# Kernel optimization log

Measured on AMD Instinct MI355X. Metric: run time of the kernel, lower is better.

## Reference

```python
import jax, jax.numpy as jnp
import numpy as np

N, E, G, P = 65536, 1048576, 512, 128   # nodes, edges, graphs, nodes per graph
K = 64                                   # sort-pool k (fixed in module)
NUM_CLASSES = 10
FEAT = 128


def _gcn_conv(x, W, b, src, dst):
    # PyG GCNConv: linear, add self-loops, symmetric-normalized aggregation, bias
    h = x @ W
    deg = jnp.ones((N,), x.dtype).at[dst].add(1.0)       # self-loop + in-degree
    dinv = jax.lax.rsqrt(deg)
    coef = (dinv[src] * dinv[dst])[:, None]
    agg = jax.ops.segment_sum(h[src] * coef, dst, num_segments=N)
    agg = agg + h * (dinv * dinv)[:, None]               # self-loop messages
    return agg + b


def setup_inputs() -> dict:
    key = jax.random.key(0)
    ks = jax.random.split(key, 12)
    x = jax.random.normal(ks[0], (N, FEAT), jnp.float32)
    src = jax.random.randint(ks[1], (E,), 0, N, dtype=jnp.int32)
    off = jax.random.randint(ks[2], (E,), 0, P, dtype=jnp.int32)
    dst = (src // P) * P + off                           # keep edges intra-graph
    edge_index = jnp.stack([src, dst])
    # balanced batch vector (implicit): node n belongs to graph n // P
    def lin(k, i, o):
        return jax.random.normal(k, (i, o), jnp.float32) / np.float32(np.sqrt(i))
    return {
        "x": x,
        "W1": lin(ks[3], FEAT, 128), "b1": jnp.zeros((128,), jnp.float32),
        "W2": lin(ks[4], 128, 64),   "b2": jnp.zeros((64,), jnp.float32),
        "W3": lin(ks[5], 64, 32),    "b3": jnp.zeros((32,), jnp.float32),
        "W4": lin(ks[6], 32, 32),    "b4": jnp.zeros((32,), jnp.float32),
        "W5": lin(ks[7], 256, 16).T, "b5": jnp.zeros((16,), jnp.float32),   # Conv1d(1,16,256,256)
        "W6": jax.random.normal(ks[8], (32, 16, 5), jnp.float32) * 0.1,      # Conv1d(16,32,5) OIH
        "b6": jnp.zeros((32,), jnp.float32),
        "Wf1": lin(ks[9], 896, 128), "bf1": jnp.zeros((128,), jnp.float32),
        "Wf2": lin(ks[10], 128, NUM_CLASSES), "bf2": jnp.zeros((NUM_CLASSES,), jnp.float32),
        "edge_index": edge_index,
    }


def reference(x, W1, b1, W2, b2, W3, b3, W4, b4, W5, b5, W6, b6,
              Wf1, bf1, Wf2, bf2, edge_index):
    src, dst = edge_index[0], edge_index[1]
    x1 = jnp.tanh(_gcn_conv(x, W1, b1, src, dst))
    x2 = jnp.tanh(_gcn_conv(x1, W2, b2, src, dst))
    x3 = jnp.tanh(_gcn_conv(x2, W3, b3, src, dst))
    x4 = jnp.tanh(_gcn_conv(x3, W4, b4, src, dst))
    h = jnp.concatenate([x1, x2, x3, x4], axis=-1)       # [N, 256]
    C = h.shape[-1]
    # global_sort_pool: balanced graphs of P nodes -> sort desc by last channel, take top-K
    hg = h.reshape(G, P, C)
    order = jnp.argsort(-hg[:, :, -1], axis=1)[:, :K]    # [G, K]
    pooled = jnp.take_along_axis(hg, order[:, :, None], axis=1)   # [G, K, C]
    # Conv1d(1, 16, 256, stride=256): kernel == stride == C, so per-node matmul
    z = jnp.einsum('gtj,cj->gct', pooled, W5) + b5[None, :, None]  # [G,16,64]
    z = jax.nn.relu(z)
    z = z.reshape(G, 16, -1, 2).max(axis=-1)                       # MaxPool1d(2,2) -> [G,16,32]
    z = jax.lax.conv_general_dilated(z, W6, (1,), 'VALID',
                                     dimension_numbers=('NCH', 'OIH', 'NCH'))
    z = jax.nn.relu(z + b6[None, :, None])                          # [G,32,28]
    z = z.reshape(G, -1)                                            # [G,896]
    out = jax.nn.relu(z @ Wf1 + bf1)
    # dropout is identity at eval time
    return jax.nn.log_softmax(out @ Wf2 + bf2, axis=-1)
```

## Files before the change

kernel.cpp:

```cpp
#include <hip/hip_runtime.h>

#define N_EDGES 1048576
#define N_GRAPH 512
#define REG     2560
#define MAXE    2560
#define PAD     64
#define CHUNK   4096

typedef __attribute__((ext_vector_type(4))) float floatx4;
typedef __attribute__((ext_vector_type(4))) int intx4;

__global__ void zero_kernel(unsigned* __restrict__ p, int n) {
    int i = blockIdx.x * blockDim.x + threadIdx.x;
    if (i < n) p[i] = 0u;
}

__global__ void scatter1p_kernel(const int* __restrict__ src, const int* __restrict__ dst,
                                 unsigned* __restrict__ cnt, unsigned short* __restrict__ ebuf) {
    __shared__ unsigned lhist[512];
    __shared__ unsigned lbase[512];
    int t = threadIdx.x;
    lhist[t] = 0; lhist[t + 256] = 0;
    __syncthreads();
    const intx4* s4 = (const intx4*)(src + blockIdx.x * CHUNK);
    const intx4* d4 = (const intx4*)(dst + blockIdx.x * CHUNK);
    unsigned gg[16]; unsigned short pk[16]; unsigned rr[16];
    int m = 0;
    for (int i = t; i < CHUNK / 4; i += 256) {
        intx4 sv = s4[i], dv = d4[i];
        int ss[4] = {sv.x, sv.y, sv.z, sv.w};
        int dd[4] = {dv.x, dv.y, dv.z, dv.w};
#pragma unroll
        for (int j = 0; j < 4; ++j) {
            unsigned g = ((unsigned)dd[j]) >> 7;
            gg[m] = g;
            pk[m] = (unsigned short)((ss[j] & 127) | ((dd[j] & 127) << 8));
            rr[m] = atomicAdd(&lhist[g], 1u);
            ++m;
        }
    }
    __syncthreads();
    lbase[t]       = lhist[t]       ? atomicAdd(&cnt[(size_t)t * PAD],         lhist[t])       : 0u;
    lbase[t + 256] = lhist[t + 256] ? atomicAdd(&cnt[(size_t)(t + 256) * PAD], lhist[t + 256]) : 0u;
    __syncthreads();
#pragma unroll
    for (int j = 0; j < 16; ++j) {
        unsigned pos = lbase[gg[j]] + rr[j];
        if (pos < REG) ebuf[(size_t)gg[j] * REG + pos] = pk[j];
    }
}

template<int CIN, int COUT>
__device__ void gcn_layer(const float* Xin, float* Xio,
                          const float* __restrict__ W, const float* __restrict__ Bv,
                          const float* __restrict__ dinv, const int* __restrict__ offs,
                          const unsigned char* __restrict__ csr,
                          const float* __restrict__ ecoef, int tid)
{
    constexpr int CL  = COUT / 4;
    constexpr int NPT = CL / 8;
    const int grp = tid / CL, cl = tid % CL;

    float acc[NPT][4];
#pragma unroll
    for (int ni = 0; ni < NPT; ++ni)
#pragma unroll
        for (int j = 0; j < 4; ++j) acc[ni][j] = 0.f;

    for (int k = 0; k < CIN; k += 4) {
        floatx4 xv[NPT];
#pragma unroll
        for (int ni = 0; ni < NPT; ++ni)
            xv[ni] = *(const floatx4*)(Xin + (grp * NPT + ni) * CIN + k);
#pragma unroll
        for (int i = 0; i < 4; ++i) {
            floatx4 wv = *(const floatx4*)(W + (k + i) * COUT + cl * 4);
#pragma unroll
            for (int ni = 0; ni < NPT; ++ni)
#pragma unroll
                for (int j = 0; j < 4; ++j)
                    acc[ni][j] += xv[ni][i] * wv[j];
        }
    }
    __syncthreads();
#pragma unroll
    for (int ni = 0; ni < NPT; ++ni) {
        floatx4 v; v[0] = acc[ni][0]; v[1] = acc[ni][1]; v[2] = acc[ni][2]; v[3] = acc[ni][3];
        *(floatx4*)(Xio + (grp * NPT + ni) * COUT + cl * 4) = v;
    }
    __syncthreads();

    floatx4 bv = *(const floatx4*)(Bv + cl * 4);
    float vout[NPT][4];
#pragma unroll
    for (int ni = 0; ni < NPT; ++ni) {
        int n = grp * NPT + ni;
        float dn = dinv[n];
        float a[4] = {0.f, 0.f, 0.f, 0.f};
        int o0 = offs[n], o1 = offs[n + 1];
        for (int p = o0; p < o1; ++p) {
            int s = csr[p] & 127;
            float cf = ecoef[p];
            floatx4 h = *(const floatx4*)(Xio + s * COUT + cl * 4);
#pragma unroll
            for (int j = 0; j < 4; ++j) a[j] += h[j] * cf;
        }
        float dnn = dn * dn;
#pragma unroll
        for (int j = 0; j < 4; ++j) {
            float t2 = a[j] + acc[ni][j] * dnn + bv[j];
            t2 = tanhf(t2);
            vout[ni][j] = fminf(fmaxf(t2, -1.0f), 1.0f);
        }
    }
    __syncthreads();
#pragma unroll
    for (int ni = 0; ni < NPT; ++ni) {
        floatx4 v; v[0] = vout[ni][0]; v[1] = vout[ni][1]; v[2] = vout[ni][2]; v[3] = vout[ni][3];
        *(floatx4*)(Xio + (grp * NPT + ni) * COUT + cl * 4) = v;
    }
    __syncthreads();
}

__global__ __launch_bounds__(1024, 1) void mega_kernel(
    const float* __restrict__ x,
    const float* __restrict__ W1, const float* __restrict__ b1,
    const float* __restrict__ W2, const float* __restrict__ b2,
    const float* __restrict__ W3, const float* __restrict__ b3,
    const float* __restrict__ W4, const float* __restrict__ b4,
    const float* __restrict__ W5, const float* __restrict__ b5,
    const float* __restrict__ W6, const float* __restrict__ b6,
    const float* __restrict__ Wf1, const float* __restrict__ bf1,
    const float* __restrict__ Wf2, const float* __restrict__ bf2,
    const unsigned* __restrict__ cnt, const unsigned short* __restrict__ ebuf,
    float* __restrict__ out)
{
    __shared__ __align__(16) char pool[157952];
    int*   ldeg = (int*)(pool + 0);
    int*   offs = (int*)(pool + 512);
    float* dinv = (float*)(pool + 1040);
    float* key  = (float*)(pool + 1552);
    unsigned short* ord = (unsigned short*)(pool + 2064);
    unsigned char*  csr = (unsigned char*)(pool + 2304);
    float* ecoef = (float*)(pool + 2304 + 2560 + 16);
    float* W5s   = (float*)(pool + 2304);
    float* X1   = (float*)(pool + 18688);
    float* X2   = (float*)(pool + 84224);
    float* X3   = (float*)(pool + 116992);
    float* X4   = (float*)(pool + 133376);
    float* SCR  = (float*)(pool + 149760);
    float* Zs   = SCR;
    float* ZMP  = SCR + 1024;
    float* Z896 = SCR;
    float* PART = SCR + 1024;
    float* FC1  = SCR + 896;
    float* LG   = SCR;

    const int g   = blockIdx.x;
    const int tid = threadIdx.x;
    int cnt_g = (int)cnt[(size_t)g * PAD];
    if (cnt_g > MAXE) cnt_g = MAXE;
    const unsigned short* eg = ebuf + (size_t)g * REG;

    unsigned short ev[3]; int ne = 0;
    for (int e = tid; e < cnt_g; e += 1024) ev[ne++] = eg[e];

    if (tid < 128) ldeg[tid] = 0;
    __syncthreads();
    for (int i = 0; i < ne; ++i) atomicAdd(&ldeg[(ev[i] >> 8) & 127], 1);
    __syncthreads();
    if (tid < 128) offs[tid + 1] = ldeg[tid];
    if (tid == 0)  offs[0] = 0;
    __syncthreads();
    for (int d = 1; d < 128; d <<= 1) {
        int v = 0;
        if (tid < 128 && tid >= d) v = offs[tid + 1 - d];
        __syncthreads();
        if (tid < 128 && tid >= d) offs[tid + 1] += v;
        __syncthreads();
    }
    if (tid < 128) {
        dinv[tid] = 1.0f / sqrtf((float)(1 + ldeg[tid]));
        ldeg[tid] = offs[tid];
    }
    __syncthreads();
    for (int i = 0; i < ne; ++i) {
        int dn_ = (ev[i] >> 8) & 127, sn = ev[i] & 127;
        int p = atomicAdd(&ldeg[dn_], 1);
        csr[p]   = (unsigned char)sn;
        ecoef[p] = dinv[sn] * dinv[dn_];
    }
    const float* xg = x + (size_t)g * 16384;
    for (int idx = tid; idx < 4096; idx += 1024)
        *(floatx4*)(X1 + idx * 4) = *(const floatx4*)(xg + idx * 4);
    __syncthreads();

    gcn_layer<128, 128>(X1, X1, W1, b1, dinv, offs, csr, ecoef, tid);
    gcn_layer<128,  64>(X1, X2, W2, b2, dinv, offs, csr, ecoef, tid);
    gcn_layer< 64,  32>(X2, X3, W3, b3, dinv, offs, csr, ecoef, tid);
    gcn_layer< 32,  32>(X3, X4, W4, b4, dinv, offs, csr, ecoef, tid);

    if (tid < 128) key[tid] = X4[tid * 32 + 31];
    if (tid < 64)  ord[tid] = (unsigned short)tid;
    __syncthreads();
    for (int idx = tid; idx < 4096; idx += 1024) W5s[idx] = W5[idx];
    __syncthreads();
    if (tid < 128) {
        float myk = key[tid];
        int r = 0;
        for (int j = 0; j < 128; ++j) {
            float kj = key[j];
            r += (kj > myk) || (kj == myk && j < tid);
        }
        if (r < 64) ord[r] = (unsigned short)tid;
    }
    __syncthreads();

    {
        int q = tid >> 6, t = tid & 63;
        int node = ord[t] & 127;
        float z0 = b5[q];
        const float* w5a = W5s + q * 256;
        floatx4 zv = {0.f, 0.f, 0.f, 0.f};
        for (int jj = 0; jj < 32; ++jj) {
            int j = (jj + t) & 31;
            floatx4 pv = *(const floatx4*)(X1 + node * 128 + j * 4);
            floatx4 wv = *(const floatx4*)(w5a + j * 4);
#pragma unroll
            for (int u = 0; u < 4; ++u) zv[u] += pv[u] * wv[u];
        }
        for (int jj = 0; jj < 16; ++jj) {
            int j = (jj + t) & 15;
            floatx4 pv = *(const floatx4*)(X2 + node * 64 + j * 4);
            floatx4 wv = *(const floatx4*)(w5a + 128 + j * 4);
#pragma unroll
            for (int u = 0; u < 4; ++u) zv[u] += pv[u] * wv[u];
        }
        for (int jj = 0; jj < 8; ++jj) {
            int j = (jj + t) & 7;
            floatx4 pv = *(const floatx4*)(X3 + node * 32 + j * 4);
            floatx4 wv = *(const floatx4*)(w5a + 192 + j * 4);
#pragma unroll
            for (int u = 0; u < 4; ++u) zv[u] += pv[u] * wv[u];
        }
        for (int jj = 0; jj < 8; ++jj) {
            int j = (jj + t) & 7;
            floatx4 pv = *(const floatx4*)(X4 + node * 32 + j * 4);
            floatx4 wv = *(const floatx4*)(w5a + 224 + j * 4);
#pragma unroll
            for (int u = 0; u < 4; ++u) zv[u] += pv[u] * wv[u];
        }
        z0 += zv[0] + zv[1] + zv[2] + zv[3];
        Zs[q * 64 + t] = fmaxf(z0, 0.f);
    }
    __syncthreads();
    if (tid < 512) {
        int c = tid >> 5, p = tid & 31;
        ZMP[c * 32 + p] = fmaxf(Zs[c * 64 + 2 * p], Zs[c * 64 + 2 * p + 1]);
    }
    __syncthreads();
    for (int idx = tid; idx < 2560; idx += 1024) W5s[idx] = W6[idx];
    __syncthreads();
    if (tid < 896) {
        int oc = tid / 28, p = tid % 28;
        float s = b6[oc];
#pragma unroll
        for (int i = 0; i < 16; ++i) {
            const float* wrow = W5s + (oc * 16 + i) * 5;
#pragma unroll
            for (int k = 0; k < 5; ++k)
                s += ZMP[i * 32 + p + k] * wrow[k];
        }
        Z896[tid] = fmaxf(s, 0.f);
    }
    __syncthreads();
    {
        int f = tid & 127, q = tid >> 7;
        float s = 0.f;
        for (int i = q * 112; i < (q + 1) * 112; ++i)
            s += Z896[i] * Wf1[i * 128 + f];
        PART[q * 128 + f] = s;
    }
    __syncthreads();
    if (tid < 128) {
        float s = bf1[tid];
#pragma unroll
        for (int q = 0; q < 8; ++q) s += PART[q * 128 + tid];
        FC1[tid] = fmaxf(s, 0.f);
    }
    __syncthreads();
    if (tid < 10) {
        float s = bf2[tid];
        for (int i = 0; i < 128; ++i) s += FC1[i] * Wf2[i * 10 + tid];
        LG[tid] = s;
    }
    __syncthreads();
    if (tid == 0) {
        float mx = LG[0];
        for (int i = 1; i < 10; ++i) mx = fmaxf(mx, LG[i]);
        float se = 0.f;
        for (int i = 0; i < 10; ++i) se += expf(LG[i] - mx);
        LG[16] = mx + logf(se);
    }
    __syncthreads();
    if (tid < 10)
        out[g * 10 + tid] = LG[tid] - LG[16];
}

extern "C" void kernel_launch(void* const* d_in, const int* in_sizes, int n_in,
                              void* d_out, int out_size, void* d_ws, size_t ws_size,
                              hipStream_t stream) {
    (void)in_sizes; (void)n_in; (void)out_size; (void)ws_size;
    const float* x   = (const float*)d_in[0];
    const float* W1  = (const float*)d_in[1];
    const float* b1  = (const float*)d_in[2];
    const float* W2  = (const float*)d_in[3];
    const float* b2  = (const float*)d_in[4];
    const float* W3  = (const float*)d_in[5];
    const float* b3  = (const float*)d_in[6];
    const float* W4  = (const float*)d_in[7];
    const float* b4  = (const float*)d_in[8];
    const float* W5  = (const float*)d_in[9];
    const float* b5  = (const float*)d_in[10];
    const float* W6  = (const float*)d_in[11];
    const float* b6  = (const float*)d_in[12];
    const float* Wf1 = (const float*)d_in[13];
    const float* bf1 = (const float*)d_in[14];
    const float* Wf2 = (const float*)d_in[15];
    const float* bf2 = (const float*)d_in[16];
    const int* ei  = (const int*)d_in[17];
    const int* src = ei;
    const int* dst = ei + N_EDGES;

    char* ws = (char*)d_ws;
    unsigned* cnt         = (unsigned*)(ws);
    unsigned short* ebuf  = (unsigned short*)(ws + 131072);

    zero_kernel<<<32, 1024, 0, stream>>>(cnt, 512 * PAD);
    scatter1p_kernel<<<N_EDGES / CHUNK, 256, 0, stream>>>(src, dst, cnt, ebuf);
    mega_kernel<<<N_GRAPH, 1024, 0, stream>>>(x, W1, b1, W2, b2, W3, b3, W4, b4,
                                              W5, b5, W6, b6, Wf1, bf1, Wf2, bf2,
                                              cnt, ebuf, (float*)d_out);
}
```

Before: 285.3 us.

## Split GCN layer into matmul and agg phases, stage scatter writes in LDS

The scatter kernel now processes smaller chunks, does a local prefix scan per chunk, and stages packed edges in shared memory so the global writes to the per-graph edge buffers go out grouped by graph. In the mega kernel each GCN layer is split into a matmul phase and an aggregation phase. Aggregation is remapped so each thread owns one node and a contiguous channel slice, and the edge coefficient and source index are packed into a single float2 load. This is meant to cut scattered global stores and balance per-thread aggregation work. The cost is more shared memory and more barriers, and some threads sit idle in the narrow aggregation layers.

```diff
diff --git a/kernel.cpp b/kernel.cpp
--- a/kernel.cpp
+++ b/kernel.cpp
@@ -5,9 +5,11 @@
 #define REG     2560
 #define MAXE    2560
 #define PAD     64
-#define CHUNK   4096
+#define CHUNK   2048
+#define SBLK    (N_EDGES / CHUNK)
 
 typedef __attribute__((ext_vector_type(4))) float floatx4;
+typedef __attribute__((ext_vector_type(2))) float floatx2;
 typedef __attribute__((ext_vector_type(4))) int intx4;
 
 __global__ void zero_kernel(unsigned* __restrict__ p, int n) {
@@ -15,50 +17,66 @@
     if (i < n) p[i] = 0u;
 }
 
-__global__ void scatter1p_kernel(const int* __restrict__ src, const int* __restrict__ dst,
-                                 unsigned* __restrict__ cnt, unsigned short* __restrict__ ebuf) {
+__global__ void scatter_kernel(const int* __restrict__ src, const int* __restrict__ dst,
+                               unsigned* __restrict__ cnt, unsigned short* __restrict__ ebuf) {
+    __shared__ unsigned short sbuf[CHUNK];
+    __shared__ unsigned short sg[CHUNK];
     __shared__ unsigned lhist[512];
-    __shared__ unsigned lbase[512];
-    int t = threadIdx.x;
+    __shared__ unsigned lscan[512];
+    __shared__ unsigned gbase[512];
+    const int t = threadIdx.x;
     lhist[t] = 0; lhist[t + 256] = 0;
     __syncthreads();
-    const intx4* s4 = (const intx4*)(src + blockIdx.x * CHUNK);
-    const intx4* d4 = (const intx4*)(dst + blockIdx.x * CHUNK);
-    unsigned gg[16]; unsigned short pk[16]; unsigned rr[16];
-    int m = 0;
-    for (int i = t; i < CHUNK / 4; i += 256) {
-        intx4 sv = s4[i], dv = d4[i];
+    const intx4* s4 = (const intx4*)(src + blockIdx.x * CHUNK) + t * 2;
+    const intx4* d4 = (const intx4*)(dst + blockIdx.x * CHUNK) + t * 2;
+    unsigned short gg[8], pk[8], rr[8];
+#pragma unroll
+    for (int h = 0; h < 2; ++h) {
+        intx4 sv = s4[h], dv = d4[h];
         int ss[4] = {sv.x, sv.y, sv.z, sv.w};
         int dd[4] = {dv.x, dv.y, dv.z, dv.w};
 #pragma unroll
         for (int j = 0; j < 4; ++j) {
             unsigned g = ((unsigned)dd[j]) >> 7;
-            gg[m] = g;
-            pk[m] = (unsigned short)((ss[j] & 127) | ((dd[j] & 127) << 8));
-            rr[m] = atomicAdd(&lhist[g], 1u);
-            ++m;
-        }
-    }
-    __syncthreads();
-    lbase[t]       = lhist[t]       ? atomicAdd(&cnt[(size_t)t * PAD],         lhist[t])       : 0u;
-    lbase[t + 256] = lhist[t + 256] ? atomicAdd(&cnt[(size_t)(t + 256) * PAD], lhist[t + 256]) : 0u;
-    __syncthreads();
-#pragma unroll
-    for (int j = 0; j < 16; ++j) {
-        unsigned pos = lbase[gg[j]] + rr[j];
-        if (pos < REG) ebuf[(size_t)gg[j] * REG + pos] = pk[j];
+            gg[h * 4 + j] = (unsigned short)g;
+            pk[h * 4 + j] = (unsigned short)((ss[j] & 127) | ((dd[j] & 127) << 8));
+            rr[h * 4 + j] = (unsigned short)atomicAdd(&lhist[g], 1u);
+        }
+    }
+    __syncthreads();
+    unsigned a0 = lhist[t], a1 = lhist[t + 256];
+    lscan[t] = a0; lscan[t + 256] = a1;
+    __syncthreads();
+    for (int d = 1; d < 512; d <<= 1) {
+        unsigned v0 = (t >= d) ? lscan[t - d] : 0u;
+        unsigned v1 = (t + 256 >= d) ? lscan[t + 256 - d] : 0u;
+        __syncthreads();
+        lscan[t] += v0; lscan[t + 256] += v1;
+        __syncthreads();
+    }
+    lscan[t] -= a0; lscan[t + 256] -= a1;
+    gbase[t]       = a0 ? atomicAdd(&cnt[(size_t)t * PAD], a0)         : 0u;
+    gbase[t + 256] = a1 ? atomicAdd(&cnt[(size_t)(t + 256) * PAD], a1) : 0u;
+    __syncthreads();
+#pragma unroll
+    for (int j = 0; j < 8; ++j) {
+        unsigned pos = lscan[gg[j]] + rr[j];
+        sbuf[pos] = pk[j]; sg[pos] = gg[j];
+    }
+    __syncthreads();
+    for (int i = t; i < CHUNK; i += 256) {
+        unsigned g = sg[i];
+        unsigned pos = gbase[g] + (i - lscan[g]);
+        if (pos < REG) ebuf[(size_t)g * REG + pos] = sbuf[i];
     }
 }
 
 template<int CIN, int COUT>
-__device__ void gcn_layer(const float* Xin, float* Xio,
-                          const float* __restrict__ W, const float* __restrict__ Bv,
-                          const float* __restrict__ dinv, const int* __restrict__ offs,
-                          const unsigned char* __restrict__ csr,
-                          const float* __restrict__ ecoef, int tid)
+__device__ void gcn_matmul(const float* Xin, float* Xio,
+                           const float* __restrict__ W, int tid)
 {
     constexpr int CL  = COUT / 4;
-    constexpr int NPT = CL / 8;
+    constexpr int NPT = 128 / (1024 / CL);
     const int grp = tid / CL, cl = tid % CL;
 
     float acc[NPT][4];
@@ -89,35 +107,58 @@
         *(floatx4*)(Xio + (grp * NPT + ni) * COUT + cl * 4) = v;
     }
     __syncthreads();
-
-    floatx4 bv = *(const floatx4*)(Bv + cl * 4);
-    float vout[NPT][4];
-#pragma unroll
-    for (int ni = 0; ni < NPT; ++ni) {
-        int n = grp * NPT + ni;
-        float dn = dinv[n];
-        float a[4] = {0.f, 0.f, 0.f, 0.f};
-        int o0 = offs[n], o1 = offs[n + 1];
+}
+
+template<int COUT, int CPT>
+__device__ void gcn_agg(float* Xio, const float* __restrict__ Bv,
+                        const float* __restrict__ dinv, const int* __restrict__ offs,
+                        const float* __restrict__ epack, int tid)
+{
+    constexpr int TPN = COUT / CPT;
+    constexpr int TOT = 128 * TPN;
+    constexpr int NV  = CPT / 4;
+    float v[NV][4];
+    if (tid < TOT) {
+        const int n = tid / TPN, cb = (tid % TPN) * CPT;
+        float a[NV][4];
+#pragma unroll
+        for (int q = 0; q < NV; ++q)
+#pragma unroll
+            for (int j = 0; j < 4; ++j) a[q][j] = 0.f;
+        const int o0 = offs[n], o1 = offs[n + 1];
         for (int p = o0; p < o1; ++p) {
-            int s = csr[p] & 127;
-            float cf = ecoef[p];
-            floatx4 h = *(const floatx4*)(Xio + s * COUT + cl * 4);
-#pragma unroll
-            for (int j = 0; j < 4; ++j) a[j] += h[j] * cf;
-        }
-        float dnn = dn * dn;
-#pragma unroll
-        for (int j = 0; j < 4; ++j) {
-            float t2 = a[j] + acc[ni][j] * dnn + bv[j];
-            t2 = tanhf(t2);
-            vout[ni][j] = fminf(fmaxf(t2, -1.0f), 1.0f);
-        }
-    }
-    __syncthreads();
-#pragma unroll
-    for (int ni = 0; ni < NPT; ++ni) {
-        floatx4 v; v[0] = vout[ni][0]; v[1] = vout[ni][1]; v[2] = vout[ni][2]; v[3] = vout[ni][3];
-        *(floatx4*)(Xio + (grp * NPT + ni) * COUT + cl * 4) = v;
+            floatx2 e = *(const floatx2*)(epack + 2 * p);
+            float cf = e[0];
+            int s = (int)__float_as_uint(e[1]);
+            const float* hr = Xio + s * COUT + cb;
+#pragma unroll
+            for (int q = 0; q < NV; ++q) {
+                floatx4 h = *(const floatx4*)(hr + q * 4);
+#pragma unroll
+                for (int j = 0; j < 4; ++j) a[q][j] += h[j] * cf;
+            }
+        }
+        float dn = dinv[n], dnn = dn * dn;
+#pragma unroll
+        for (int q = 0; q < NV; ++q) {
+            floatx4 hs = *(const floatx4*)(Xio + n * COUT + cb + q * 4);
+            floatx4 bv = *(const floatx4*)(Bv + cb + q * 4);
+#pragma unroll
+            for (int j = 0; j < 4; ++j) {
+                float t2 = a[q][j] + hs[j] * dnn + bv[j];
+                t2 = tanhf(t2);
+                v[q][j] = fminf(fmaxf(t2, -1.0f), 1.0f);
+            }
+        }
+    }
+    __syncthreads();
+    if (tid < TOT) {
+        const int n = tid / TPN, cb = (tid % TPN) * CPT;
+#pragma unroll
+        for (int q = 0; q < NV; ++q) {
+            floatx4 o; o[0] = v[q][0]; o[1] = v[q][1]; o[2] = v[q][2]; o[3] = v[q][3];
+            *(floatx4*)(Xio + n * COUT + cb + q * 4) = o;
+        }
     }
     __syncthreads();
 }
@@ -135,20 +176,19 @@
     const unsigned* __restrict__ cnt, const unsigned short* __restrict__ ebuf,
     float* __restrict__ out)
 {
-    __shared__ __align__(16) char pool[157952];
+    __shared__ __align__(16) char pool[162048];
     int*   ldeg = (int*)(pool + 0);
     int*   offs = (int*)(pool + 512);
     float* dinv = (float*)(pool + 1040);
     float* key  = (float*)(pool + 1552);
     unsigned short* ord = (unsigned short*)(pool + 2064);
-    unsigned char*  csr = (unsigned char*)(pool + 2304);
-    float* ecoef = (float*)(pool + 2304 + 2560 + 16);
+    float* epack = (float*)(pool + 2304);
     float* W5s   = (float*)(pool + 2304);
-    float* X1   = (float*)(pool + 18688);
-    float* X2   = (float*)(pool + 84224);
-    float* X3   = (float*)(pool + 116992);
-    float* X4   = (float*)(pool + 133376);
-    float* SCR  = (float*)(pool + 149760);
+    float* X1   = (float*)(pool + 22784);
+    float* X2   = (float*)(pool + 88320);
+    float* X3   = (float*)(pool + 121088);
+    float* X4   = (float*)(pool + 137472);
+    float* SCR  = (float*)(pool + 153856);
     float* Zs   = SCR;
     float* ZMP  = SCR + 1024;
     float* Z896 = SCR;
@@ -187,18 +227,22 @@
     for (int i = 0; i < ne; ++i) {
         int dn_ = (ev[i] >> 8) & 127, sn = ev[i] & 127;
         int p = atomicAdd(&ldeg[dn_], 1);
-        csr[p]   = (unsigned char)sn;
-        ecoef[p] = dinv[sn] * dinv[dn_];
+        floatx2 e; e[0] = dinv[sn] * dinv[dn_]; e[1] = __uint_as_float((unsigned)sn);
+        *(floatx2*)(epack + 2 * p) = e;
     }
     const float* xg = x + (size_t)g * 16384;
     for (int idx = tid; idx < 4096; idx += 1024)
         *(floatx4*)(X1 + idx * 4) = *(const floatx4*)(xg + idx * 4);
     __syncthreads();
 
-    gcn_layer<128, 128>(X1, X1, W1, b1, dinv, offs, csr, ecoef, tid);
-    gcn_layer<128,  64>(X1, X2, W2, b2, dinv, offs, csr, ecoef, tid);
-    gcn_layer< 64,  32>(X2, X3, W3, b3, dinv, offs, csr, ecoef, tid);
-    gcn_layer< 32,  32>(X3, X4, W4, b4, dinv, offs, csr, ecoef, tid);
+    gcn_matmul<128, 128>(X1, X1, W1, tid);
+    gcn_agg<128, 16>(X1, b1, dinv, offs, epack, tid);
+    gcn_matmul<128,  64>(X1, X2, W2, tid);
+    gcn_agg< 64,  8>(X2, b2, dinv, offs, epack, tid);
+    gcn_matmul< 64,  32>(X2, X3, W3, tid);
+    gcn_agg< 32,  8>(X3, b3, dinv, offs, epack, tid);
+    gcn_matmul< 32,  32>(X3, X4, W4, tid);
+    gcn_agg< 32,  8>(X4, b4, dinv, offs, epack, tid);
 
     if (tid < 128) key[tid] = X4[tid * 32 + 31];
     if (tid < 64)  ord[tid] = (unsigned short)tid;
@@ -337,7 +381,7 @@
     unsigned short* ebuf  = (unsigned short*)(ws + 131072);
 
     zero_kernel<<<32, 1024, 0, stream>>>(cnt, 512 * PAD);
-    scatter1p_kernel<<<N_EDGES / CHUNK, 256, 0, stream>>>(src, dst, cnt, ebuf);
+    scatter_kernel<<<SBLK, 256, 0, stream>>>(src, dst, cnt, ebuf);
     mega_kernel<<<N_GRAPH, 1024, 0, stream>>>(x, W1, b1, W2, b2, W3, b3, W4, b4,
                                               W5, b5, W6, b6, Wf1, bf1, Wf2, bf2,
                                               cnt, ebuf, (float*)d_out);
```

Result: slower. 298.4 us (+4.6%).
